# Kernel optimization log

Hardware: AMD Instinct MI355X
Metric: run time of the kernel (lower is better)

The kernel has to match this reference:

```python
import jax, jax.numpy as jnp
import numpy as np

K = 3        # num_nextn_predict_layers (draft tokens per step)
B = 64       # batch of generation requests
V = 128000   # vocab
H = 7168     # hidden_size
MAXR = 128   # max_num_requests (pool slots)


def setup_inputs() -> dict:
    key = jax.random.key(0)
    ks = jax.random.split(key, 6)
    return {
        "logits": jax.random.normal(ks[0], (B * (K + 1), V), jnp.float32),
        "hidden_states": jax.random.normal(ks[1], (B * (K + 1), H), jnp.float32),
        "draft_tokens": jax.random.randint(ks[2], (B, K), 0, V, jnp.int32),
        "slot_ids": jnp.arange(B, dtype=jnp.int32),  # unique slots per request
        "past_hidden_pool": jax.random.normal(ks[3], (MAXR, K, H), jnp.float32),
        "past_tokens_pool": jax.random.randint(ks[4], (MAXR, K), 0, V, jnp.int32),
        "draft_logits": jax.random.normal(ks[5], (B, K, V), jnp.float32),
    }


def reference(logits, hidden_states, draft_tokens, slot_ids,
              past_hidden_pool, past_tokens_pool, draft_logits):
    # --- sample_and_accept_draft_tokens (greedy) ---
    # target model produced K+1 logits per generation request
    target_tokens = jnp.argmax(logits.reshape(B, K + 1, V), axis=-1).astype(jnp.int32)  # [B,K+1]
    match = (target_tokens[:, :K] == draft_tokens).astype(jnp.int32)                    # [B,K]
    prefix = jnp.cumprod(match, axis=1)            # accept only a matching prefix
    num_accepted = 1 + jnp.sum(prefix, axis=1)     # [B] in [1, K+1]
    accepted_tokens = target_tokens                # [B,K+1]; first num_accepted are valid

    # --- update_mtp_hidden_states: slot-based gather/scatter into pools ---
    hidden = hidden_states.reshape(B, K + 1, H)
    # keep the last K of concat(old_past_K, newly_accepted_n) per request
    comb_h = jnp.concatenate([past_hidden_pool[slot_ids], hidden], axis=1)      # [B,2K+1,H]
    comb_t = jnp.concatenate([past_tokens_pool[slot_ids], accepted_tokens], axis=1)  # [B,2K+1]
    gidx = num_accepted[:, None] + jnp.arange(K, dtype=jnp.int32)[None, :]       # [B,K]
    new_h = jnp.take_along_axis(comb_h, gidx[:, :, None], axis=1)                # [B,K,H]
    new_t = jnp.take_along_axis(comb_t, gidx, axis=1)                            # [B,K]
    new_hidden_pool = past_hidden_pool.at[slot_ids].set(new_h)
    new_tokens_pool = past_tokens_pool.at[slot_ids].set(new_t)

    # --- draft_sampler over MTP-layer logits ---
    next_draft_tokens = jnp.argmax(draft_logits, axis=-1).astype(jnp.int32)      # [B,K]

    # next_new_tokens = [last accepted token, next drafts]
    last = jnp.take_along_axis(accepted_tokens, (num_accepted - 1)[:, None], axis=1)  # [B,1]
    next_new_tokens = jnp.concatenate([last, next_draft_tokens], axis=1)         # [B,K+1]

    return (logits, accepted_tokens, num_accepted, next_draft_tokens,
            next_new_tokens, new_hidden_pool, new_tokens_pool)
```

## Files before the change

kernel.cpp:

```cpp
#include <hip/hip_runtime.h>

#define KK 3
#define BB 64
#define VV 128000
#define HH 7168
#define MAXR 128
#define NROWS (BB * (KK + 1) + BB * KK)
#define SEG 5
#define UNROLL 5

typedef float f4 __attribute__((ext_vector_type(4)));

static constexpr size_t OFF_ACC = (size_t)BB * (KK + 1) * VV;
static constexpr size_t OFF_NUM = OFF_ACC + (size_t)BB * (KK + 1);
static constexpr size_t OFF_ND  = OFF_NUM + BB;
static constexpr size_t OFF_NN  = OFF_ND + (size_t)BB * KK;
static constexpr size_t OFF_HP  = OFF_NN + (size_t)BB * (KK + 1);
static constexpr size_t OFF_TP  = OFF_HP + (size_t)MAXR * KK * HH;

__device__ __forceinline__ void scan4(const f4& v, int base, float& best, int& bidx) {
    if (v.x > best) { best = v.x; bidx = base; }
    if (v.y > best) { best = v.y; bidx = base + 1; }
    if (v.z > best) { best = v.z; bidx = base + 2; }
    if (v.w > best) { best = v.w; bidx = base + 3; }
}

__global__ __launch_bounds__(256) void argmax_partial_copy_kernel(
    const float* __restrict__ logits,
    const float* __restrict__ draft_logits,
    float* __restrict__ out_logits,
    int* __restrict__ ws_pidx,
    float* __restrict__ ws_pval)
{
    const int seg = blockIdx.x;
    const int row = blockIdx.y;
    const int tid = threadIdx.x;
    const bool is_target = (row < BB * (KK + 1));

    const float* srcf = is_target ? (logits + (size_t)row * VV)
                                  : (draft_logits + (size_t)(row - BB * (KK + 1)) * VV);
    const f4* src4 = reinterpret_cast<const f4*>(srcf);
    f4* dst4 = is_target
        ? reinterpret_cast<f4*>(out_logits + (size_t)row * VV)
        : nullptr;

    float best = -__builtin_huge_valf();
    int bidx = 0;
    const int base = seg * 6400;

    #pragma unroll 1
    for (int it = 0; it < 5; ++it) {
        const int i0 = base + it * (UNROLL * 256) + tid;
        f4 v0 = src4[i0];
        f4 v1 = src4[i0 + 256];
        f4 v2 = src4[i0 + 512];
        f4 v3 = src4[i0 + 768];
        f4 v4 = src4[i0 + 1024];
        __builtin_amdgcn_sched_barrier(0);
        scan4(v0, i0 * 4, best, bidx);
        scan4(v1, (i0 + 256) * 4, best, bidx);
        scan4(v2, (i0 + 512) * 4, best, bidx);
        scan4(v3, (i0 + 768) * 4, best, bidx);
        scan4(v4, (i0 + 1024) * 4, best, bidx);
        if (is_target) {
            __builtin_nontemporal_store(v0, dst4 + i0);
            __builtin_nontemporal_store(v1, dst4 + i0 + 256);
            __builtin_nontemporal_store(v2, dst4 + i0 + 512);
            __builtin_nontemporal_store(v3, dst4 + i0 + 768);
            __builtin_nontemporal_store(v4, dst4 + i0 + 1024);
        }
    }

    #pragma unroll
    for (int off = 32; off > 0; off >>= 1) {
        const float ov = __shfl_xor(best, off, 64);
        const int   oi = __shfl_xor(bidx, off, 64);
        if (ov > best || (ov == best && oi < bidx)) { best = ov; bidx = oi; }
    }

    __shared__ float swv[4];
    __shared__ int   swi[4];
    if ((tid & 63) == 0) { swv[tid >> 6] = best; swi[tid >> 6] = bidx; }
    __syncthreads();
    if (tid == 0) {
        #pragma unroll
        for (int w = 1; w < 4; ++w) {
            if (swv[w] > best || (swv[w] == best && swi[w] < bidx)) {
                best = swv[w]; bidx = swi[w];
            }
        }
        ws_pidx[row * SEG + seg] = bidx;
        ws_pval[row * SEG + seg] = best;
    }
}

__global__ __launch_bounds__(512) void logic_kernel(
    const int* __restrict__ draft_tokens,
    const int* __restrict__ slot_ids,
    const int* __restrict__ past_tokens_pool,
    const int* __restrict__ ws_pidx,
    const float* __restrict__ ws_pval,
    float* __restrict__ out,
    int* __restrict__ ws_numacc,
    int* __restrict__ ws_inv)
{
    __shared__ int s_am[NROWS];
    __shared__ int s_numacc[BB];
    __shared__ int s_inv[MAXR];

    const int tid = threadIdx.x;

    if (tid < NROWS) {
        float best = ws_pval[tid * SEG];
        int bidx = ws_pidx[tid * SEG];
        #pragma unroll
        for (int s = 1; s < SEG; ++s) {
            const float v = ws_pval[tid * SEG + s];
            const int   i = ws_pidx[tid * SEG + s];
            if (v > best || (v == best && i < bidx)) { best = v; bidx = i; }
        }
        s_am[tid] = bidx;
    }
    if (tid < MAXR) s_inv[tid] = -1;
    __syncthreads();
    if (tid < BB) s_inv[slot_ids[tid]] = tid;

    if (tid < BB) {
        int t[KK + 1];
        #pragma unroll
        for (int k = 0; k <= KK; ++k) t[k] = s_am[tid * (KK + 1) + k];

        int na = 1;
        #pragma unroll
        for (int k = 0; k < KK; ++k) {
            if (t[k] == draft_tokens[tid * KK + k] && na == k + 1) na++;
        }
        s_numacc[tid] = na;
        ws_numacc[tid] = na;

        #pragma unroll
        for (int k = 0; k <= KK; ++k)
            out[OFF_ACC + tid * (KK + 1) + k] = (float)t[k];
        out[OFF_NUM + tid] = (float)na;

        int nd[KK];
        #pragma unroll
        for (int k = 0; k < KK; ++k) {
            nd[k] = s_am[BB * (KK + 1) + tid * KK + k];
            out[OFF_ND + tid * KK + k] = (float)nd[k];
        }
        out[OFF_NN + tid * (KK + 1)] = (float)t[na - 1];
        #pragma unroll
        for (int k = 0; k < KK; ++k)
            out[OFF_NN + tid * (KK + 1) + 1 + k] = (float)nd[k];
    }
    __syncthreads();

    if (tid < MAXR) {
        const int b = s_inv[tid];
        ws_inv[tid] = b;
        if (b < 0) {
            #pragma unroll
            for (int k = 0; k < KK; ++k)
                out[OFF_TP + tid * KK + k] = (float)past_tokens_pool[tid * KK + k];
        } else {
            const int na = s_numacc[b];
            #pragma unroll
            for (int k = 0; k < KK; ++k) {
                const int src = na + k;
                const int v = (src < KK)
                    ? past_tokens_pool[tid * KK + src]
                    : s_am[b * (KK + 1) + (src - KK)];
                out[OFF_TP + tid * KK + k] = (float)v;
            }
        }
    }
}

#define HSPLIT 4
__global__ __launch_bounds__(256) void hidden_pool_kernel(
    const float* __restrict__ hidden_states,
    const float* __restrict__ past_hidden_pool,
    const int* __restrict__ ws_numacc,
    const int* __restrict__ ws_inv,
    float* __restrict__ out_hp)
{
    const int rowid = blockIdx.x / HSPLIT;
    const int q     = blockIdx.x % HSPLIT;
    const int slot = rowid / KK;
    const int k = rowid - slot * KK;
    const int b = ws_inv[slot];

    const float* src;
    if (b < 0) {
        src = past_hidden_pool + (size_t)rowid * HH;
    } else {
        const int srcrow = ws_numacc[b] + k;
        src = (srcrow < KK)
            ? past_hidden_pool + ((size_t)slot * KK + srcrow) * HH
            : hidden_states + ((size_t)b * (KK + 1) + (srcrow - KK)) * HH;
    }

    const f4* s4 = reinterpret_cast<const f4*>(src);
    f4* d4 = reinterpret_cast<f4*>(out_hp + (size_t)rowid * HH);
    const int n4 = HH / 4;
    const int per = n4 / HSPLIT;
    const int lo = q * per;
    for (int i = lo + threadIdx.x; i < lo + per; i += 256) {
        f4 v = s4[i];
        __builtin_nontemporal_store(v, d4 + i);
    }
}

extern "C" void kernel_launch(void* const* d_in, const int* in_sizes, int n_in,
                              void* d_out, int out_size, void* d_ws, size_t ws_size,
                              hipStream_t stream) {
    const float* logits           = (const float*)d_in[0];
    const float* hidden_states    = (const float*)d_in[1];
    const int*   draft_tokens     = (const int*)d_in[2];
    const int*   slot_ids         = (const int*)d_in[3];
    const float* past_hidden_pool = (const float*)d_in[4];
    const int*   past_tokens_pool = (const int*)d_in[5];
    const float* draft_logits     = (const float*)d_in[6];

    float* out = (float*)d_out;

    int* wsI = (int*)d_ws;
    int*   ws_pidx   = wsI;
    float* ws_pval   = (float*)(wsI + NROWS * SEG);
    int*   ws_numacc = wsI + 2 * NROWS * SEG;
    int*   ws_inv    = ws_numacc + BB;

    dim3 grid1(SEG, NROWS);
    argmax_partial_copy_kernel<<<grid1, 256, 0, stream>>>(
        logits, draft_logits, out, ws_pidx, ws_pval);

    logic_kernel<<<1, 512, 0, stream>>>(
        draft_tokens, slot_ids, past_tokens_pool, ws_pidx, ws_pval,
        out, ws_numacc, ws_inv);

    hidden_pool_kernel<<<MAXR * KK * HSPLIT, 256, 0, stream>>>(
        hidden_states, past_hidden_pool, ws_numacc, ws_inv, out + OFF_HP);
}
```

Before: 68.72 us.

## Use fixed persistent grid over fine segments with per-wave argmax partials

Replaces the 2D grid (5 segments per row) with a fixed grid of 2048 blocks, each walking a contiguous range of 5x finer segments across rows. Each segment is reduced only within a wave, and each wave writes its own partial, so the block-level shared-memory reduction and __syncthreads are gone. The aim is to balance work across CUs and avoid tail effects in the memory-bound scan/copy. The cost is that the single-block logic kernel now serially reduces 100 partials per row instead of 5.

```diff
diff --git a/kernel.cpp b/kernel.cpp
--- a/kernel.cpp
+++ b/kernel.cpp
@@ -6,8 +6,10 @@
 #define HH 7168
 #define MAXR 128
 #define NROWS (BB * (KK + 1) + BB * KK)
-#define SEG 5
-#define UNROLL 5
+#define SEG 25
+#define NSEG (NROWS * SEG)
+#define NBLK 2048
+#define BIGB (NSEG - NBLK * (NSEG / NBLK))
 
 typedef float f4 __attribute__((ext_vector_type(4)));
 
@@ -32,31 +34,32 @@
     int* __restrict__ ws_pidx,
     float* __restrict__ ws_pval)
 {
-    const int seg = blockIdx.x;
-    const int row = blockIdx.y;
+    const int b   = blockIdx.x;
     const int tid = threadIdx.x;
-    const bool is_target = (row < BB * (KK + 1));
-
-    const float* srcf = is_target ? (logits + (size_t)row * VV)
-                                  : (draft_logits + (size_t)(row - BB * (KK + 1)) * VV);
-    const f4* src4 = reinterpret_cast<const f4*>(srcf);
-    f4* dst4 = is_target
-        ? reinterpret_cast<f4*>(out_logits + (size_t)row * VV)
-        : nullptr;
-
-    float best = -__builtin_huge_valf();
-    int bidx = 0;
-    const int base = seg * 6400;
-
-    #pragma unroll 1
-    for (int it = 0; it < 5; ++it) {
-        const int i0 = base + it * (UNROLL * 256) + tid;
+    const int nseg_mine = (b < BIGB) ? (NSEG / NBLK + 1) : (NSEG / NBLK);
+    const int seg0 = (b < BIGB) ? b * (NSEG / NBLK + 1)
+                                : BIGB * (NSEG / NBLK + 1) + (b - BIGB) * (NSEG / NBLK);
+
+    for (int s = seg0; s < seg0 + nseg_mine; ++s) {
+        const int row = (unsigned)s / SEG;
+        const int sub = s - row * SEG;
+        const bool is_target = (row < BB * (KK + 1));
+
+        const float* srcf = is_target
+            ? (logits + (size_t)row * VV)
+            : (draft_logits + (size_t)(row - BB * (KK + 1)) * VV);
+        const f4* src4 = reinterpret_cast<const f4*>(srcf);
+        f4* dst4 = reinterpret_cast<f4*>(out_logits + (size_t)row * VV);
+
+        const int i0 = sub * 1280 + tid;
         f4 v0 = src4[i0];
         f4 v1 = src4[i0 + 256];
         f4 v2 = src4[i0 + 512];
         f4 v3 = src4[i0 + 768];
         f4 v4 = src4[i0 + 1024];
         __builtin_amdgcn_sched_barrier(0);
+        float best = -__builtin_huge_valf();
+        int bidx = 0;
         scan4(v0, i0 * 4, best, bidx);
         scan4(v1, (i0 + 256) * 4, best, bidx);
         scan4(v2, (i0 + 512) * 4, best, bidx);
@@ -69,28 +72,18 @@
             __builtin_nontemporal_store(v3, dst4 + i0 + 768);
             __builtin_nontemporal_store(v4, dst4 + i0 + 1024);
         }
-    }
-
-    #pragma unroll
-    for (int off = 32; off > 0; off >>= 1) {
-        const float ov = __shfl_xor(best, off, 64);
-        const int   oi = __shfl_xor(bidx, off, 64);
-        if (ov > best || (ov == best && oi < bidx)) { best = ov; bidx = oi; }
-    }
-
-    __shared__ float swv[4];
-    __shared__ int   swi[4];
-    if ((tid & 63) == 0) { swv[tid >> 6] = best; swi[tid >> 6] = bidx; }
-    __syncthreads();
-    if (tid == 0) {
-        #pragma unroll
-        for (int w = 1; w < 4; ++w) {
-            if (swv[w] > best || (swv[w] == best && swi[w] < bidx)) {
-                best = swv[w]; bidx = swi[w];
-            }
-        }
-        ws_pidx[row * SEG + seg] = bidx;
-        ws_pval[row * SEG + seg] = best;
+
+        #pragma unroll
+        for (int off = 32; off > 0; off >>= 1) {
+            const float ov = __shfl_xor(best, off, 64);
+            const int   oi = __shfl_xor(bidx, off, 64);
+            if (ov > best || (ov == best && oi < bidx)) { best = ov; bidx = oi; }
+        }
+        if ((tid & 63) == 0) {
+            const int p = s * 4 + (tid >> 6);
+            ws_pidx[p] = bidx;
+            ws_pval[p] = best;
+        }
     }
 }
 
@@ -111,12 +104,12 @@
     const int tid = threadIdx.x;
 
     if (tid < NROWS) {
-        float best = ws_pval[tid * SEG];
-        int bidx = ws_pidx[tid * SEG];
-        #pragma unroll
-        for (int s = 1; s < SEG; ++s) {
-            const float v = ws_pval[tid * SEG + s];
-            const int   i = ws_pidx[tid * SEG + s];
+        const int base = tid * SEG * 4;
+        float best = ws_pval[base];
+        int bidx = ws_pidx[base];
+        for (int j = 1; j < SEG * 4; ++j) {
+            const float v = ws_pval[base + j];
+            const int   i = ws_pidx[base + j];
             if (v > best || (v == best && i < bidx)) { best = v; bidx = i; }
         }
         s_am[tid] = bidx;
@@ -227,12 +220,11 @@
 
     int* wsI = (int*)d_ws;
     int*   ws_pidx   = wsI;
-    float* ws_pval   = (float*)(wsI + NROWS * SEG);
-    int*   ws_numacc = wsI + 2 * NROWS * SEG;
+    float* ws_pval   = (float*)(wsI + NSEG * 4);
+    int*   ws_numacc = wsI + 2 * NSEG * 4;
     int*   ws_inv    = ws_numacc + BB;
 
-    dim3 grid1(SEG, NROWS);
-    argmax_partial_copy_kernel<<<grid1, 256, 0, stream>>>(
+    argmax_partial_copy_kernel<<<NBLK, 256, 0, stream>>>(
         logits, draft_logits, out, ws_pidx, ws_pval);
 
     logic_kernel<<<1, 512, 0, stream>>>(
```

Result: slower. 117.5 us (+70.9%).

## Fuse single-block logic kernel into hidden-pool copy kernel to drop a launch

Applied to the files above, without the earlier changes.

Removes the serial single-block logic kernel and folds its work into the pool-copy kernel. Each copy block now finds its own request slot with a ballot over slot_ids and recomputes num_accepted from the partial argmax workspace. One extra block writes the per-request token outputs. This removes one kernel launch and the serialization on a one-block kernel, at the cost of redundant small argmax/accept work in every pool block plus two extra block barriers.

```diff
diff --git a/kernel.cpp b/kernel.cpp
--- a/kernel.cpp
+++ b/kernel.cpp
@@ -8,6 +8,8 @@
 #define NROWS (BB * (KK + 1) + BB * KK)
 #define SEG 5
 #define UNROLL 5
+#define HSPLIT 4
+#define NPOOLBLK (MAXR * KK * HSPLIT)
 
 typedef float f4 __attribute__((ext_vector_type(4)));
 
@@ -23,6 +25,19 @@
     if (v.y > best) { best = v.y; bidx = base + 1; }
     if (v.z > best) { best = v.z; bidx = base + 2; }
     if (v.w > best) { best = v.w; bidx = base + 3; }
+}
+
+__device__ __forceinline__ void vimax(float v, int i, float& best, int& bidx) {
+    if (v > best || (v == best && i < bidx)) { best = v; bidx = i; }
+}
+
+__device__ __forceinline__ int row_argmax(const int* ws_pidx, const float* ws_pval, int row) {
+    const int base = row * SEG;
+    float best = ws_pval[base];
+    int bidx = ws_pidx[base];
+    #pragma unroll
+    for (int s = 1; s < SEG; ++s) vimax(ws_pval[base + s], ws_pidx[base + s], best, bidx);
+    return bidx;
 }
 
 __global__ __launch_bounds__(256) void argmax_partial_copy_kernel(
@@ -75,7 +90,7 @@
     for (int off = 32; off > 0; off >>= 1) {
         const float ov = __shfl_xor(best, off, 64);
         const int   oi = __shfl_xor(bidx, off, 64);
-        if (ov > best || (ov == best && oi < bidx)) { best = ov; bidx = oi; }
+        vimax(ov, oi, best, bidx);
     }
 
     __shared__ float swv[4];
@@ -84,129 +99,117 @@
     __syncthreads();
     if (tid == 0) {
         #pragma unroll
-        for (int w = 1; w < 4; ++w) {
-            if (swv[w] > best || (swv[w] == best && swi[w] < bidx)) {
-                best = swv[w]; bidx = swi[w];
-            }
-        }
+        for (int w = 1; w < 4; ++w) vimax(swv[w], swi[w], best, bidx);
         ws_pidx[row * SEG + seg] = bidx;
         ws_pval[row * SEG + seg] = best;
     }
 }
 
-__global__ __launch_bounds__(512) void logic_kernel(
+__global__ __launch_bounds__(256) void pool_logic_kernel(
+    const float* __restrict__ hidden_states,
+    const float* __restrict__ past_hidden_pool,
     const int* __restrict__ draft_tokens,
     const int* __restrict__ slot_ids,
     const int* __restrict__ past_tokens_pool,
     const int* __restrict__ ws_pidx,
     const float* __restrict__ ws_pval,
-    float* __restrict__ out,
-    int* __restrict__ ws_numacc,
-    int* __restrict__ ws_inv)
+    float* __restrict__ out)
 {
-    __shared__ int s_am[NROWS];
-    __shared__ int s_numacc[BB];
-    __shared__ int s_inv[MAXR];
-
     const int tid = threadIdx.x;
 
-    if (tid < NROWS) {
-        float best = ws_pval[tid * SEG];
-        int bidx = ws_pidx[tid * SEG];
-        #pragma unroll
-        for (int s = 1; s < SEG; ++s) {
-            const float v = ws_pval[tid * SEG + s];
-            const int   i = ws_pidx[tid * SEG + s];
-            if (v > best || (v == best && i < bidx)) { best = v; bidx = i; }
-        }
-        s_am[tid] = bidx;
-    }
-    if (tid < MAXR) s_inv[tid] = -1;
-    __syncthreads();
-    if (tid < BB) s_inv[slot_ids[tid]] = tid;
-
-    if (tid < BB) {
-        int t[KK + 1];
-        #pragma unroll
-        for (int k = 0; k <= KK; ++k) t[k] = s_am[tid * (KK + 1) + k];
-
-        int na = 1;
-        #pragma unroll
-        for (int k = 0; k < KK; ++k) {
-            if (t[k] == draft_tokens[tid * KK + k] && na == k + 1) na++;
-        }
-        s_numacc[tid] = na;
-        ws_numacc[tid] = na;
-
-        #pragma unroll
-        for (int k = 0; k <= KK; ++k)
-            out[OFF_ACC + tid * (KK + 1) + k] = (float)t[k];
-        out[OFF_NUM + tid] = (float)na;
-
-        int nd[KK];
-        #pragma unroll
-        for (int k = 0; k < KK; ++k) {
-            nd[k] = s_am[BB * (KK + 1) + tid * KK + k];
-            out[OFF_ND + tid * KK + k] = (float)nd[k];
-        }
-        out[OFF_NN + tid * (KK + 1)] = (float)t[na - 1];
-        #pragma unroll
-        for (int k = 0; k < KK; ++k)
-            out[OFF_NN + tid * (KK + 1) + 1 + k] = (float)nd[k];
-    }
-    __syncthreads();
-
-    if (tid < MAXR) {
-        const int b = s_inv[tid];
-        ws_inv[tid] = b;
-        if (b < 0) {
+    if (blockIdx.x == NPOOLBLK) {
+        __shared__ int s_t[BB * (KK + 1)];
+        __shared__ int s_d[BB * KK];
+
+        s_t[tid] = row_argmax(ws_pidx, ws_pval, tid);
+        if (tid < BB * KK)
+            s_d[tid] = row_argmax(ws_pidx, ws_pval, BB * (KK + 1) + tid);
+        __syncthreads();
+
+        if (tid < BB) {
+            int t[KK + 1];
+            #pragma unroll
+            for (int k = 0; k <= KK; ++k) t[k] = s_t[tid * (KK + 1) + k];
+
+            int na = 1;
             #pragma unroll
             for (int k = 0; k < KK; ++k)
-                out[OFF_TP + tid * KK + k] = (float)past_tokens_pool[tid * KK + k];
-        } else {
-            const int na = s_numacc[b];
+                if (t[k] == draft_tokens[tid * KK + k] && na == k + 1) na++;
+
+            #pragma unroll
+            for (int k = 0; k <= KK; ++k)
+                out[OFF_ACC + tid * (KK + 1) + k] = (float)t[k];
+            out[OFF_NUM + tid] = (float)na;
+
+            int nd[KK];
             #pragma unroll
             for (int k = 0; k < KK; ++k) {
-                const int src = na + k;
-                const int v = (src < KK)
-                    ? past_tokens_pool[tid * KK + src]
-                    : s_am[b * (KK + 1) + (src - KK)];
-                out[OFF_TP + tid * KK + k] = (float)v;
+                nd[k] = s_d[tid * KK + k];
+                out[OFF_ND + tid * KK + k] = (float)nd[k];
             }
-        }
-    }
-}
-
-#define HSPLIT 4
-__global__ __launch_bounds__(256) void hidden_pool_kernel(
-    const float* __restrict__ hidden_states,
-    const float* __restrict__ past_hidden_pool,
-    const int* __restrict__ ws_numacc,
-    const int* __restrict__ ws_inv,
-    float* __restrict__ out_hp)
-{
+            out[OFF_NN + tid * (KK + 1)] = (float)t[na - 1];
+            #pragma unroll
+            for (int k = 0; k < KK; ++k)
+                out[OFF_NN + tid * (KK + 1) + 1 + k] = (float)nd[k];
+        }
+        return;
+    }
+
     const int rowid = blockIdx.x / HSPLIT;
     const int q     = blockIdx.x % HSPLIT;
-    const int slot = rowid / KK;
-    const int k = rowid - slot * KK;
-    const int b = ws_inv[slot];
+    const int slot  = rowid / KK;
+    const int k     = rowid - slot * KK;
+
+    __shared__ int s_b, s_na, s_tok[KK + 1];
+
+    if (tid < 64) {
+        const bool hit = (slot_ids[tid] == slot);
+        const unsigned long long m = __ballot(hit);
+        const int b = (int)__ffsll((long long)m) - 1;
+        if (tid == 0) s_b = b;
+        if (b >= 0) {
+            if (tid < KK + 1)
+                s_tok[tid] = row_argmax(ws_pidx, ws_pval, b * (KK + 1) + tid);
+        }
+    }
+    __syncthreads();
+
+    const int b = s_b;
+    int na = 1;
+    if (b >= 0 && tid == 0) {
+        #pragma unroll
+        for (int kk2 = 0; kk2 < KK; ++kk2)
+            if (s_tok[kk2] == draft_tokens[b * KK + kk2] && na == kk2 + 1) na++;
+        s_na = na;
+    }
+    __syncthreads();
 
     const float* src;
     if (b < 0) {
         src = past_hidden_pool + (size_t)rowid * HH;
+        if (q == 0 && tid < KK)
+            out[OFF_TP + rowid + tid - k + k] ,
+            out[OFF_TP + slot * KK + tid] = (float)past_tokens_pool[slot * KK + tid];
     } else {
-        const int srcrow = ws_numacc[b] + k;
+        na = s_na;
+        const int srcrow = na + k;
         src = (srcrow < KK)
             ? past_hidden_pool + ((size_t)slot * KK + srcrow) * HH
             : hidden_states + ((size_t)b * (KK + 1) + (srcrow - KK)) * HH;
+        if (q == 0 && tid < KK) {
+            const int sr = na + tid;
+            const int v = (sr < KK) ? past_tokens_pool[slot * KK + sr]
+                                    : s_tok[sr - KK];
+            out[OFF_TP + slot * KK + tid] = (float)v;
+        }
     }
 
     const f4* s4 = reinterpret_cast<const f4*>(src);
-    f4* d4 = reinterpret_cast<f4*>(out_hp + (size_t)rowid * HH);
+    f4* d4 = reinterpret_cast<f4*>(out + OFF_HP + (size_t)rowid * HH);
     const int n4 = HH / 4;
     const int per = n4 / HSPLIT;
     const int lo = q * per;
-    for (int i = lo + threadIdx.x; i < lo + per; i += 256) {
+    for (int i = lo + tid; i < lo + per; i += 256) {
         f4 v = s4[i];
         __builtin_nontemporal_store(v, d4 + i);
     }
@@ -226,19 +229,14 @@
     float* out = (float*)d_out;
 
     int* wsI = (int*)d_ws;
-    int*   ws_pidx   = wsI;
-    float* ws_pval   = (float*)(wsI + NROWS * SEG);
-    int*   ws_numacc = wsI + 2 * NROWS * SEG;
-    int*   ws_inv    = ws_numacc + BB;
+    int*   ws_pidx = wsI;
+    float* ws_pval = (float*)(wsI + NROWS * SEG);
 
     dim3 grid1(SEG, NROWS);
     argmax_partial_copy_kernel<<<grid1, 256, 0, stream>>>(
         logits, draft_logits, out, ws_pidx, ws_pval);
 
-    logic_kernel<<<1, 512, 0, stream>>>(
-        draft_tokens, slot_ids, past_tokens_pool, ws_pidx, ws_pval,
-        out, ws_numacc, ws_inv);
-
-    hidden_pool_kernel<<<MAXR * KK * HSPLIT, 256, 0, stream>>>(
-        hidden_states, past_hidden_pool, ws_numacc, ws_inv, out + OFF_HP);
-}
+    pool_logic_kernel<<<NPOOLBLK + 1, 256, 0, stream>>>(
+        hidden_states, past_hidden_pool, draft_tokens, slot_ids,
+        past_tokens_pool, ws_pidx, ws_pval, out);
+}
```

After: 66.41 us. 3.4% less time.
